# Kernel optimization log

Hardware: AMD Instinct MI355X
Metric: run time of the kernel (lower is better)

The kernel has to match this reference:

```python
import jax, jax.numpy as jnp
import numpy as np
import math

B, S, H, D = 8, 4096, 768, 64  # batch, seq_len, hidden_dim, head_size


def setup_inputs() -> dict:
    key = jax.random.key(0)
    kx, kk, kq, kv, kbk, kbq, kbv = jax.random.split(key, 7)
    s = 1.0 / math.sqrt(H)
    return {
        "x": jax.random.normal(kx, (B, S, H), dtype=jnp.float32),
        "Wk": jax.random.normal(kk, (H, D), dtype=jnp.float32) * s,
        "bk": jax.random.normal(kbk, (D,), dtype=jnp.float32) * s,
        "Wq": jax.random.normal(kq, (H, D), dtype=jnp.float32) * s,
        "bq": jax.random.normal(kbq, (D,), dtype=jnp.float32) * s,
        "Wv": jax.random.normal(kv, (H, D), dtype=jnp.float32) * s,
        "bv": jax.random.normal(kbv, (D,), dtype=jnp.float32) * s,
    }


def reference(x, Wk, bk, Wq, bq, Wv, bv):
    # projections: [B, S, D]
    k = x @ Wk + bk
    q = x @ Wq + bq
    v = x @ Wv + bv
    # full O(S^2) attention scores, as in the original module
    weight = jnp.einsum("bqd,bkd->bqk", q, k)  # [B, S, S]
    causal = jnp.tril(jnp.ones((S, S), dtype=bool))
    # original masks first, then divides by sqrt(head_size); -inf/sqrt = -inf
    weight = jnp.where(causal, weight, -jnp.inf) / math.sqrt(D)
    weight = jax.nn.softmax(weight, axis=-1)
    # dropout p=0.0 (eval-mode reference): identity
    out = jnp.einsum("bqk,bkd->bqd", weight, v)  # [B, S, D]
    return out
```

## Files before the change

### kernel.cpp

```cpp
#include <hip/hip_runtime.h>
#include <hip/hip_bf16.h>
#include <math.h>

#define B_ 8
#define S_ 4096
#define H_ 768
#define D_ 64

typedef __bf16 bf16;
typedef bf16 bf16x8 __attribute__((ext_vector_type(8)));
typedef bf16 bf16x4 __attribute__((ext_vector_type(4)));
typedef float floatx4 __attribute__((ext_vector_type(4)));
typedef short short4v __attribute__((ext_vector_type(4)));

#define S_WAITCNT_VM(N) asm volatile("s_waitcnt vmcnt(" #N ")" ::: "memory")
#define S_BARRIER()     asm volatile("s_barrier" ::: "memory")

__device__ __forceinline__ floatx4 mfma16(bf16x4 a, bf16x4 b, floatx4 c) {
#if __has_builtin(__builtin_amdgcn_mfma_f32_16x16x16_bf16)
    return __builtin_amdgcn_mfma_f32_16x16x16_bf16(a, b, c, 0, 0, 0);
#elif __has_builtin(__builtin_amdgcn_mfma_f32_16x16x16bf16_1k)
    return __builtin_amdgcn_mfma_f32_16x16x16bf16_1k(
        __builtin_bit_cast(short4v, a), __builtin_bit_cast(short4v, b), c, 0, 0, 0);
#else
    asm volatile("v_mfma_f32_16x16x16_bf16 %0, %1, %2, %0"
                 : "+v"(c) : "v"(a), "v"(b));
    return c;
#endif
}

__device__ __forceinline__ int sw_off(int r, int chunk) {
    return r * 128 + ((chunk ^ (r & 7)) << 4);
}
__device__ __forceinline__ int sw_elem(int r, int e) {
    return r * 64 + (((e >> 3) ^ (r & 7)) << 3) + (e & 7);
}

__device__ __forceinline__ void dma16(const void* gsrc, void* ldst) {
    __builtin_amdgcn_global_load_lds(
        (const __attribute__((address_space(1))) unsigned int*)gsrc,
        (__attribute__((address_space(3))) unsigned int*)ldst,
        16, 0, 0);
}

__global__ __launch_bounds__(256) void wtrans_kernel(
    const float* __restrict__ Wq, const float* __restrict__ Wk,
    const float* __restrict__ Wv, bf16* __restrict__ wt)
{
    __shared__ bf16 t_lds[64][72];
    const float* W = (blockIdx.y == 0) ? Wq : (blockIdx.y == 1) ? Wk : Wv;
    bf16* o = wt + ((size_t)blockIdx.y * 12 + blockIdx.x) * 4096;
    const int k0 = blockIdx.x * 64;
    const int tid = threadIdx.x;
    #pragma unroll
    for (int rep = 0; rep < 16; ++rep) {
        int idx = rep * 256 + tid;
        int r = idx >> 6, n = idx & 63;
        t_lds[n][r] = (bf16)W[(size_t)(k0 + r) * D_ + n];
    }
    __syncthreads();
    #pragma unroll
    for (int rep = 0; rep < 16; ++rep) {
        int idx = rep * 256 + tid;
        int n = idx >> 6, kk = idx & 63;
        o[sw_elem(n, kk)] = t_lds[n][kk];
    }
}

__global__ __launch_bounds__(256, 2) void proj_kernel(
    const float* __restrict__ x, const bf16* __restrict__ wt,
    const float* __restrict__ bq, const float* __restrict__ bk,
    const float* __restrict__ bv,
    bf16* __restrict__ qout, bf16* __restrict__ kout, bf16* __restrict__ vtt)
{
    __shared__ bf16  wlds[2][3][4096];
    __shared__ float xlds[2][4096];

    const int tid  = threadIdx.x;
    const int lane = tid & 63;
    const int wave = tid >> 6;
    const int quad = lane >> 4;
    const int c    = lane & 15;
    const int m0   = blockIdx.x * 64;

    auto stageAll = [&](int kt, int buf) {
        #pragma unroll
        for (int w = 0; w < 3; ++w) {
            const bf16* src = wt + (size_t)(w * 12 + kt) * 4096 + wave * 1024 + lane * 8;
            bf16* dst = &wlds[buf][w][wave * 1024 + lane * 8];
            dma16(src, dst);
            dma16(src + 512, dst + 512);
        }
        #pragma unroll
        for (int rep = 0; rep < 4; ++rep) {
            const int ci  = rep * 256 + tid;
            const int row = ci >> 4;
            const int l   = (ci & 15) ^ (row & 15);
            const char* src = (const char*)x
                + ((size_t)(m0 + row) * H_ + kt * 64) * 4 + l * 16;
            dma16(src, (char*)&xlds[buf][0] + ci * 16);
        }
    };

    floatx4 acc[4][3] = {};

    stageAll(0, 0);
    stageAll(1, 1);

    for (int kt = 0; kt < 12; ++kt) {
        if (kt < 11) { S_WAITCNT_VM(10); } else { S_WAITCNT_VM(0); }
        S_BARRIER();
        const int cur = kt & 1;
        #pragma unroll
        for (int s = 0; s < 2; ++s) {
            bf16x8 bfrag[3];
            #pragma unroll
            for (int t = 0; t < 3; ++t) {
                const int g = wave * 3 + t, w = g >> 2, tn = g & 3;
                bfrag[t] = *(const bf16x8*)
                    ((const char*)&wlds[cur][w][0] + sw_off(tn * 16 + c, s * 4 + quad));
            }
            #pragma unroll
            for (int mg = 0; mg < 4; ++mg) {
                const int row = mg * 16 + c;
                const int lc  = s * 8 + quad * 2;
                const char* xb = (const char*)&xlds[cur][0] + row * 256;
                float4 f0 = *(const float4*)(xb + ((lc       ^ (row & 15)) << 4));
                float4 f1 = *(const float4*)(xb + (((lc + 1) ^ (row & 15)) << 4));
                bf16x8 af;
                af[0] = (bf16)f0.x; af[1] = (bf16)f0.y; af[2] = (bf16)f0.z; af[3] = (bf16)f0.w;
                af[4] = (bf16)f1.x; af[5] = (bf16)f1.y; af[6] = (bf16)f1.z; af[7] = (bf16)f1.w;
                #pragma unroll
                for (int t = 0; t < 3; ++t)
                    acc[mg][t] = __builtin_amdgcn_mfma_f32_16x16x32_bf16(
                        af, bfrag[t], acc[mg][t], 0, 0, 0);
            }
        }
        S_BARRIER();
        if (kt < 10) stageAll(kt + 2, cur);
    }

    const int bb = m0 >> 12;
    const int jt = (m0 & 4095) >> 6;
    const size_t tbase = ((size_t)bb * 64 + jt) * 4096;
    #pragma unroll
    for (int t = 0; t < 3; ++t) {
        const int g = wave * 3 + t, w = g >> 2, tn = g & 3;
        const int n = tn * 16 + c;
        const float bias = (w == 0 ? bq : w == 1 ? bk : bv)[n];
        #pragma unroll
        for (int mg = 0; mg < 4; ++mg) {
            const int sl0 = mg * 16 + quad * 4;
            if (w == 0) {
                #pragma unroll
                for (int r = 0; r < 4; ++r)
                    qout[(size_t)(m0 + sl0 + r) * 128 + n] = (bf16)(acc[mg][t][r] + bias);
            } else if (w == 1) {
                #pragma unroll
                for (int r = 0; r < 4; ++r)
                    kout[tbase + sw_elem(sl0 + r, n)] = (bf16)(acc[mg][t][r] + bias);
            } else {
                bf16x4 pk;
                #pragma unroll
                for (int r = 0; r < 4; ++r) pk[r] = (bf16)(acc[mg][t][r] + bias);
                *(bf16x4*)&vtt[tbase + sw_elem(n, sl0)] = pk;
            }
        }
    }
}

__global__ __launch_bounds__(128, 2) void attn_kernel(
    const bf16* __restrict__ q, const bf16* __restrict__ k,
    const bf16* __restrict__ vt, float* __restrict__ out,
    float* __restrict__ opart, float* __restrict__ lpws)
{
    __shared__ bf16 klds[2][4096];
    __shared__ bf16 vlds[2][4096];

    const int tid  = threadIdx.x;
    const int lane = tid & 63;
    const int wave = tid >> 6;
    const int quad = lane >> 4;
    const int c    = lane & 15;
    const int i    = blockIdx.x;
    const int b    = i & 7;

    int qt, j0, jend, half = 0, split = 0;
    if (i < 1024) {
        const int u = i >> 3;
        qt   = 127 - (u >> 1);
        half = u & 1;
        split = 1;
        const int jmax = qt >> 1;
        const int jmid = (jmax + 1) >> 1;
        j0   = half ? jmid : 0;
        jend = half ? jmax : (jmid - 1);
    } else {
        qt   = 63 - ((i - 1024) >> 3);
        j0   = 0;
        jend = qt >> 1;
    }
    const int jmax_diag = qt >> 1;
    const int qrow = qt * 32 + wave * 16;
    const float cl = 0.18033688011112042f;
    const float M2 = 16.0f;

    const bf16* ktile0 = k  + (size_t)b * 64 * 4096;
    const bf16* vtile0 = vt + (size_t)b * 64 * 4096;

    auto stage = [&](const bf16* gsrc, bf16* ldst) {
        const bf16* s = gsrc + wave * 2048 + lane * 8;
        bf16* d = ldst + wave * 2048;
        #pragma unroll
        for (int n = 0; n < 4; ++n) dma16(s + n * 512, d + n * 512);
    };

    bf16x8 qf[2];
    #pragma unroll
    for (int s = 0; s < 2; ++s)
        qf[s] = *(const bf16x8*)
            &q[(size_t)(b * S_ + qrow + c) * 128 + s * 32 + quad * 8];

    floatx4 acc_o[4] = {};
    floatx4 lacc = {0.f, 0.f, 0.f, 0.f};

    stage(ktile0 + (size_t)j0 * 4096, klds[j0 & 1]);
    stage(vtile0 + (size_t)j0 * 4096, vlds[j0 & 1]);
    if (j0 < jend) {
        stage(ktile0 + (size_t)(j0 + 1) * 4096, klds[(j0 + 1) & 1]);
        stage(vtile0 + (size_t)(j0 + 1) * 4096, vlds[(j0 + 1) & 1]);
    }

    #pragma unroll 1
    for (int j = j0; j <= jend; ++j) {
        if (j < jend) { S_WAITCNT_VM(8); } else { S_WAITCNT_VM(0); }
        S_BARRIER();
        const int cur = j & 1;

        floatx4 sa[4] = {};
        #pragma unroll
        for (int s = 0; s < 2; ++s)
            #pragma unroll
            for (int tn = 0; tn < 4; ++tn) {
                bf16x8 kf = *(const bf16x8*)
                    ((const char*)&klds[cur][0] + sw_off(tn * 16 + c, s * 4 + quad));
                sa[tn] = __builtin_amdgcn_mfma_f32_16x16x32_bf16(kf, qf[s], sa[tn], 0, 0, 0);
            }

        bf16x4 vfr[4][4];
        #pragma unroll
        for (int td = 0; td < 4; ++td)
            #pragma unroll
            for (int tn = 0; tn < 4; ++tn)
                vfr[td][tn] = *(const bf16x4*)
                    &vlds[cur][sw_elem(td * 16 + c, tn * 16 + quad * 4)];

        if (j == jmax_diag) {
            #pragma unroll
            for (int tn = 0; tn < 4; ++tn) {
                const int kvb = j * 64 + tn * 16 + quad * 4;
                #pragma unroll
                for (int r = 0; r < 4; ++r)
                    if (kvb + r > qrow + c) sa[tn][r] = -INFINITY;
            }
        }

        #pragma unroll
        for (int tn = 0; tn < 4; ++tn)
            #pragma unroll
            for (int r = 0; r < 4; ++r) {
                float p = __builtin_amdgcn_exp2f(fmaf(sa[tn][r], cl, -M2));
                sa[tn][r] = p;
                lacc[r] += p;
            }

        #pragma unroll
        for (int tn = 0; tn < 4; ++tn) {
            bf16x4 pb;
            #pragma unroll
            for (int r = 0; r < 4; ++r) pb[r] = (bf16)sa[tn][r];
            #pragma unroll
            for (int td = 0; td < 4; ++td)
                acc_o[td] = mfma16(vfr[td][tn], pb, acc_o[td]);
        }

        S_BARRIER();
        if (j + 2 <= jend) {
            stage(ktile0 + (size_t)(j + 2) * 4096, klds[cur]);
            stage(vtile0 + (size_t)(j + 2) * 4096, vlds[cur]);
        }
    }

    float lsum = (lacc[0] + lacc[1]) + (lacc[2] + lacc[3]);
    lsum += __shfl_xor(lsum, 16);
    lsum += __shfl_xor(lsum, 32);

    if (!split) {
        const float rl = 1.0f / lsum;
        #pragma unroll
        for (int td = 0; td < 4; ++td) {
            floatx4 v = acc_o[td] * rl;
            *(float4*)&out[(size_t)(b * S_ + qrow + c) * 64 + td * 16 + quad * 4]
                = *(float4*)&v;
        }
    } else {
        const int tile = qt - 64;
        const int row  = wave * 16 + c;
        float* op = opart + ((((size_t)half * 8 + b) * 64 + tile) * 32) * 64;
        #pragma unroll
        for (int td = 0; td < 4; ++td)
            *(float4*)&op[row * 64 + td * 16 + quad * 4] = *(float4*)&acc_o[td];
        if (quad == 0)
            lpws[(((size_t)half * 8 + b) * 64 + tile) * 32 + row] = lsum;
    }
}

__global__ __launch_bounds__(256) void combine_kernel(
    const float* __restrict__ opart, const float* __restrict__ lpws,
    float* __restrict__ out)
{
    const int b    = blockIdx.x & 7;
    const int tile = blockIdx.x >> 3;
    const int tid  = threadIdx.x;
    const int row  = tid >> 3;
    const int c8   = (tid & 7) * 8;

    const size_t ti = ((size_t)b * 64 + tile) * 32 + row;
    const float rl = 1.0f / (lpws[ti] + lpws[(size_t)8 * 64 * 32 + ti]);

    const size_t oa = (((size_t)b * 64 + tile) * 32 + row) * 64 + c8;
    const size_t ob = (size_t)8 * 64 * 32 * 64 + oa;
    const size_t oo = (size_t)(b * S_ + (64 + tile) * 32 + row) * 64 + c8;
    #pragma unroll
    for (int h = 0; h < 2; ++h) {
        float4 a = *(const float4*)&opart[oa + h * 4];
        float4 bb = *(const float4*)&opart[ob + h * 4];
        float4 o;
        o.x = (a.x + bb.x) * rl; o.y = (a.y + bb.y) * rl;
        o.z = (a.z + bb.z) * rl; o.w = (a.w + bb.w) * rl;
        *(float4*)&out[oo + h * 4] = o;
    }
}

extern "C" void kernel_launch(void* const* d_in, const int* in_sizes, int n_in,
                              void* d_out, int out_size, void* d_ws, size_t ws_size,
                              hipStream_t stream) {
    const float* x  = (const float*)d_in[0];
    const float* Wk = (const float*)d_in[1];
    const float* bk = (const float*)d_in[2];
    const float* Wq = (const float*)d_in[3];
    const float* bq = (const float*)d_in[4];
    const float* Wv = (const float*)d_in[5];
    const float* bv = (const float*)d_in[6];
    float* out = (float*)d_out;

    bf16* q_ws  = (bf16*)d_out;
    bf16* k_ws  = (bf16*)d_ws;
    bf16* vt_ws = k_ws + (size_t)B_ * S_ * D_;
    bf16* wt_ws = vt_ws + (size_t)B_ * S_ * D_;
    float* opart = (float*)(wt_ws + 3 * 12 * 4096);
    float* lpws  = opart + (size_t)2 * 8 * 64 * 32 * 64;

    wtrans_kernel<<<dim3(H_ / 64, 3), 256, 0, stream>>>(Wq, Wk, Wv, wt_ws);
    proj_kernel<<<dim3(B_ * S_ / 64), 256, 0, stream>>>(
        x, wt_ws, bq, bk, bv, q_ws, k_ws, vt_ws);
    attn_kernel<<<dim3(1536), 128, 0, stream>>>(q_ws, k_ws, vt_ws, out, opart, lpws);
    combine_kernel<<<dim3(512), 256, 0, stream>>>(opart, lpws, out);
}
```

Before: 214.5 us.

## Restructure projection kernel: 128-row tiles, x loaded straight to registers, half-K weight staging

The QKV projection kernel now processes 128 rows per block (256 blocks instead of 512), with each wave owning 32 rows and computing all 12 output column tiles for them. x is no longer staged through LDS; each lane loads its fp32 fragments directly from global memory into registers, double-buffered across k-steps. The weights are staged in two large halves (6 k-tiles each) into 144KB of LDS. This is meant to cut LDS traffic and the per-step barriers. In exchange it lowers occupancy to one block per CU, adds a serialized stall while each weight half loads, and raises register pressure.

```diff
diff --git a/kernel.cpp b/kernel.cpp
--- a/kernel.cpp
+++ b/kernel.cpp
@@ -67,104 +67,123 @@
     }
 }
 
-__global__ __launch_bounds__(256, 2) void proj_kernel(
+__global__ __launch_bounds__(256, 1) void proj_kernel(
     const float* __restrict__ x, const bf16* __restrict__ wt,
     const float* __restrict__ bq, const float* __restrict__ bk,
     const float* __restrict__ bv,
     bf16* __restrict__ qout, bf16* __restrict__ kout, bf16* __restrict__ vtt)
 {
-    __shared__ bf16  wlds[2][3][4096];
-    __shared__ float xlds[2][4096];
+    __shared__ bf16 wlds[3][6][4096];
 
     const int tid  = threadIdx.x;
     const int lane = tid & 63;
     const int wave = tid >> 6;
     const int quad = lane >> 4;
     const int c    = lane & 15;
-    const int m0   = blockIdx.x * 64;
-
-    auto stageAll = [&](int kt, int buf) {
-        #pragma unroll
-        for (int w = 0; w < 3; ++w) {
-            const bf16* src = wt + (size_t)(w * 12 + kt) * 4096 + wave * 1024 + lane * 8;
-            bf16* dst = &wlds[buf][w][wave * 1024 + lane * 8];
-            dma16(src, dst);
-            dma16(src + 512, dst + 512);
-        }
-        #pragma unroll
-        for (int rep = 0; rep < 4; ++rep) {
-            const int ci  = rep * 256 + tid;
-            const int row = ci >> 4;
-            const int l   = (ci & 15) ^ (row & 15);
-            const char* src = (const char*)x
-                + ((size_t)(m0 + row) * H_ + kt * 64) * 4 + l * 16;
-            dma16(src, (char*)&xlds[buf][0] + ci * 16);
-        }
+    const int m0   = blockIdx.x * 128;
+
+    auto stageHalf = [&](int h) {
+        #pragma unroll
+        for (int w = 0; w < 3; ++w)
+            #pragma unroll
+            for (int ks = 0; ks < 6; ++ks) {
+                const bf16* src = wt + (size_t)(w * 12 + h * 6 + ks) * 4096 + tid * 8;
+                bf16* dst = &wlds[w][ks][tid * 8];
+                dma16(src, dst);
+                dma16(src + 2048, dst + 2048);
+            }
     };
 
-    floatx4 acc[4][3] = {};
-
-    stageAll(0, 0);
-    stageAll(1, 1);
-
-    for (int kt = 0; kt < 12; ++kt) {
-        if (kt < 11) { S_WAITCNT_VM(10); } else { S_WAITCNT_VM(0); }
-        S_BARRIER();
-        const int cur = kt & 1;
+    floatx4 acc[2][3][4] = {};
+    const float* xr[2];
+    xr[0] = &x[(size_t)(m0 + wave * 32 + c) * H_ + quad * 8];
+    xr[1] = xr[0] + 16 * H_;
+
+    float4 xb[2][2][2][2];
+
+    auto loadx = [&](int kt, int pp) {
+        #pragma unroll
+        for (int rt = 0; rt < 2; ++rt)
+            #pragma unroll
+            for (int s = 0; s < 2; ++s) {
+                const float* p = xr[rt] + kt * 64 + s * 32;
+                xb[pp][rt][s][0] = *(const float4*)p;
+                xb[pp][rt][s][1] = *(const float4*)(p + 4);
+            }
+    };
+
+    auto compute = [&](int kk, int pp) {
         #pragma unroll
         for (int s = 0; s < 2; ++s) {
-            bf16x8 bfrag[3];
-            #pragma unroll
-            for (int t = 0; t < 3; ++t) {
-                const int g = wave * 3 + t, w = g >> 2, tn = g & 3;
-                bfrag[t] = *(const bf16x8*)
-                    ((const char*)&wlds[cur][w][0] + sw_off(tn * 16 + c, s * 4 + quad));
-            }
-            #pragma unroll
-            for (int mg = 0; mg < 4; ++mg) {
-                const int row = mg * 16 + c;
-                const int lc  = s * 8 + quad * 2;
-                const char* xb = (const char*)&xlds[cur][0] + row * 256;
-                float4 f0 = *(const float4*)(xb + ((lc       ^ (row & 15)) << 4));
-                float4 f1 = *(const float4*)(xb + (((lc + 1) ^ (row & 15)) << 4));
+            bf16x8 bfr[3][4];
+            #pragma unroll
+            for (int w = 0; w < 3; ++w)
+                #pragma unroll
+                for (int tn = 0; tn < 4; ++tn)
+                    bfr[w][tn] = *(const bf16x8*)
+                        ((const char*)&wlds[w][kk][0] + sw_off(tn * 16 + c, s * 4 + quad));
+            #pragma unroll
+            for (int rt = 0; rt < 2; ++rt) {
+                float4 f0 = xb[pp][rt][s][0];
+                float4 f1 = xb[pp][rt][s][1];
                 bf16x8 af;
                 af[0] = (bf16)f0.x; af[1] = (bf16)f0.y; af[2] = (bf16)f0.z; af[3] = (bf16)f0.w;
                 af[4] = (bf16)f1.x; af[5] = (bf16)f1.y; af[6] = (bf16)f1.z; af[7] = (bf16)f1.w;
                 #pragma unroll
-                for (int t = 0; t < 3; ++t)
-                    acc[mg][t] = __builtin_amdgcn_mfma_f32_16x16x32_bf16(
-                        af, bfrag[t], acc[mg][t], 0, 0, 0);
-            }
-        }
-        S_BARRIER();
-        if (kt < 10) stageAll(kt + 2, cur);
-    }
-
-    const int bb = m0 >> 12;
-    const int jt = (m0 & 4095) >> 6;
-    const size_t tbase = ((size_t)bb * 64 + jt) * 4096;
-    #pragma unroll
-    for (int t = 0; t < 3; ++t) {
-        const int g = wave * 3 + t, w = g >> 2, tn = g & 3;
-        const int n = tn * 16 + c;
-        const float bias = (w == 0 ? bq : w == 1 ? bk : bv)[n];
-        #pragma unroll
-        for (int mg = 0; mg < 4; ++mg) {
-            const int sl0 = mg * 16 + quad * 4;
-            if (w == 0) {
-                #pragma unroll
-                for (int r = 0; r < 4; ++r)
-                    qout[(size_t)(m0 + sl0 + r) * 128 + n] = (bf16)(acc[mg][t][r] + bias);
-            } else if (w == 1) {
-                #pragma unroll
-                for (int r = 0; r < 4; ++r)
-                    kout[tbase + sw_elem(sl0 + r, n)] = (bf16)(acc[mg][t][r] + bias);
-            } else {
-                bf16x4 pk;
-                #pragma unroll
-                for (int r = 0; r < 4; ++r) pk[r] = (bf16)(acc[mg][t][r] + bias);
-                *(bf16x4*)&vtt[tbase + sw_elem(n, sl0)] = pk;
-            }
+                for (int w = 0; w < 3; ++w)
+                    #pragma unroll
+                    for (int tn = 0; tn < 4; ++tn)
+                        acc[rt][w][tn] = __builtin_amdgcn_mfma_f32_16x16x32_bf16(
+                            af, bfr[w][tn], acc[rt][w][tn], 0, 0, 0);
+            }
+        }
+    };
+
+    stageHalf(0);
+    __syncthreads();
+
+    loadx(0, 0);
+    #pragma unroll
+    for (int kk = 0; kk < 6; ++kk) {
+        if (kk < 5) loadx(kk + 1, (kk + 1) & 1);
+        compute(kk, kk & 1);
+    }
+
+    __syncthreads();
+    stageHalf(1);
+    __syncthreads();
+
+    loadx(6, 0);
+    #pragma unroll
+    for (int kk = 0; kk < 6; ++kk) {
+        if (kk < 5) loadx(7 + kk, (kk + 1) & 1);
+        compute(kk, kk & 1);
+    }
+
+    #pragma unroll
+    for (int rt = 0; rt < 2; ++rt) {
+        const int grow0 = m0 + wave * 32 + rt * 16;
+        const int bb = grow0 >> 12;
+        const int jt = (grow0 & 4095) >> 6;
+        const size_t tbase = ((size_t)bb * 64 + jt) * 4096;
+        const int sl0 = (grow0 & 63) + quad * 4;
+        #pragma unroll
+        for (int tn = 0; tn < 4; ++tn) {
+            const int n = tn * 16 + c;
+            float bqv = bq[n];
+            #pragma unroll
+            for (int r = 0; r < 4; ++r)
+                qout[(size_t)(grow0 + quad * 4 + r) * 128 + n]
+                    = (bf16)(acc[rt][0][tn][r] + bqv);
+            float bkv = bk[n];
+            #pragma unroll
+            for (int r = 0; r < 4; ++r)
+                kout[tbase + sw_elem(sl0 + r, n)] = (bf16)(acc[rt][1][tn][r] + bkv);
+            float bvv = bv[n];
+            bf16x4 pk;
+            #pragma unroll
+            for (int r = 0; r < 4; ++r) pk[r] = (bf16)(acc[rt][2][tn][r] + bvv);
+            *(bf16x4*)&vtt[tbase + sw_elem(n, sl0)] = pk;
         }
     }
 }
@@ -362,7 +381,7 @@
     float* lpws  = opart + (size_t)2 * 8 * 64 * 32 * 64;
 
     wtrans_kernel<<<dim3(H_ / 64, 3), 256, 0, stream>>>(Wq, Wk, Wv, wt_ws);
-    proj_kernel<<<dim3(B_ * S_ / 64), 256, 0, stream>>>(
+    proj_kernel<<<dim3(256), 256, 0, stream>>>(
         x, wt_ws, bq, bk, bv, q_ws, k_ws, vt_ws);
     attn_kernel<<<dim3(1536), 128, 0, stream>>>(q_ws, k_ws, vt_ws, out, opart, lpws);
     combine_kernel<<<dim3(512), 256, 0, stream>>>(opart, lpws, out);
```

Result: slower. 221.7 us (+3.4%).

## Enlarge query tile to 64 rows per block with up to four-way KV split

Applied to the files above, without the earlier changes.

Each wave now handles two 16-row query groups, so every K/V tile loaded into LDS is reused across 64 query rows instead of 32, halving KV traffic per query. Work is split into KV chunks of 16 tiles (up to 4 chunks for long rows), and a reworked combine kernel sums a variable number of partials. This raises register pressure from doubled accumulators, launches fewer blocks (1280), and writes more partial-output data.

```diff
diff --git a/kernel.cpp b/kernel.cpp
--- a/kernel.cpp
+++ b/kernel.cpp
@@ -185,23 +185,16 @@
     const int i    = blockIdx.x;
     const int b    = i & 7;
 
-    int qt, j0, jend, half = 0, split = 0;
-    if (i < 1024) {
-        const int u = i >> 3;
-        qt   = 127 - (u >> 1);
-        half = u & 1;
-        split = 1;
-        const int jmax = qt >> 1;
-        const int jmid = (jmax + 1) >> 1;
-        j0   = half ? jmid : 0;
-        jend = half ? jmax : (jmid - 1);
-    } else {
-        qt   = 63 - ((i - 1024) >> 3);
-        j0   = 0;
-        jend = qt >> 1;
-    }
-    const int jmax_diag = qt >> 1;
-    const int qrow = qt * 32 + wave * 16;
+    const int u = i >> 3;
+    int qt, chunk;
+    if (u < 16)      { qt = u;                 chunk = 0; }
+    else if (u < 48) { qt = 16 + ((u - 16) >> 1); chunk = (u - 16) & 1; }
+    else if (u < 96) { qt = 32 + (u - 48) / 3;    chunk = (u - 48) % 3; }
+    else             { qt = 48 + ((u - 96) >> 2); chunk = (u - 96) & 3; }
+    const int j0    = chunk * 16;
+    const int jend  = min(qt, j0 + 15);
+    const int split = (qt >= 16);
+    const int qrow  = qt * 64 + wave * 32;
     const float cl = 0.18033688011112042f;
     const float M2 = 16.0f;
 
@@ -215,14 +208,16 @@
         for (int n = 0; n < 4; ++n) dma16(s + n * 512, d + n * 512);
     };
 
-    bf16x8 qf[2];
-    #pragma unroll
-    for (int s = 0; s < 2; ++s)
-        qf[s] = *(const bf16x8*)
-            &q[(size_t)(b * S_ + qrow + c) * 128 + s * 32 + quad * 8];
-
-    floatx4 acc_o[4] = {};
-    floatx4 lacc = {0.f, 0.f, 0.f, 0.f};
+    bf16x8 qf[2][2];
+    #pragma unroll
+    for (int mg = 0; mg < 2; ++mg)
+        #pragma unroll
+        for (int s = 0; s < 2; ++s)
+            qf[mg][s] = *(const bf16x8*)
+                &q[(size_t)(b * S_ + qrow + mg * 16 + c) * 128 + s * 32 + quad * 8];
+
+    floatx4 acc_o[2][4] = {};
+    floatx4 lacc[2] = {};
 
     stage(ktile0 + (size_t)j0 * 4096, klds[j0 & 1]);
     stage(vtile0 + (size_t)j0 * 4096, vlds[j0 & 1]);
@@ -237,14 +232,17 @@
         S_BARRIER();
         const int cur = j & 1;
 
-        floatx4 sa[4] = {};
+        floatx4 sa[2][4] = {};
         #pragma unroll
         for (int s = 0; s < 2; ++s)
             #pragma unroll
             for (int tn = 0; tn < 4; ++tn) {
                 bf16x8 kf = *(const bf16x8*)
                     ((const char*)&klds[cur][0] + sw_off(tn * 16 + c, s * 4 + quad));
-                sa[tn] = __builtin_amdgcn_mfma_f32_16x16x32_bf16(kf, qf[s], sa[tn], 0, 0, 0);
+                #pragma unroll
+                for (int mg = 0; mg < 2; ++mg)
+                    sa[mg][tn] = __builtin_amdgcn_mfma_f32_16x16x32_bf16(
+                        kf, qf[mg][s], sa[mg][tn], 0, 0, 0);
             }
 
         bf16x4 vfr[4][4];
@@ -255,34 +253,40 @@
                 vfr[td][tn] = *(const bf16x4*)
                     &vlds[cur][sw_elem(td * 16 + c, tn * 16 + quad * 4)];
 
-        if (j == jmax_diag) {
+        if (j == qt) {
+            #pragma unroll
+            for (int mg = 0; mg < 2; ++mg)
+                #pragma unroll
+                for (int tn = 0; tn < 4; ++tn) {
+                    const int kvb = j * 64 + tn * 16 + quad * 4;
+                    #pragma unroll
+                    for (int r = 0; r < 4; ++r)
+                        if (kvb + r > qrow + mg * 16 + c) sa[mg][tn][r] = -INFINITY;
+                }
+        }
+
+        #pragma unroll
+        for (int mg = 0; mg < 2; ++mg)
+            #pragma unroll
+            for (int tn = 0; tn < 4; ++tn)
+                #pragma unroll
+                for (int r = 0; r < 4; ++r) {
+                    float p = __builtin_amdgcn_exp2f(fmaf(sa[mg][tn][r], cl, -M2));
+                    sa[mg][tn][r] = p;
+                    lacc[mg][r] += p;
+                }
+
+        #pragma unroll
+        for (int mg = 0; mg < 2; ++mg)
             #pragma unroll
             for (int tn = 0; tn < 4; ++tn) {
-                const int kvb = j * 64 + tn * 16 + quad * 4;
-                #pragma unroll
-                for (int r = 0; r < 4; ++r)
-                    if (kvb + r > qrow + c) sa[tn][r] = -INFINITY;
-            }
-        }
-
-        #pragma unroll
-        for (int tn = 0; tn < 4; ++tn)
-            #pragma unroll
-            for (int r = 0; r < 4; ++r) {
-                float p = __builtin_amdgcn_exp2f(fmaf(sa[tn][r], cl, -M2));
-                sa[tn][r] = p;
-                lacc[r] += p;
-            }
-
-        #pragma unroll
-        for (int tn = 0; tn < 4; ++tn) {
-            bf16x4 pb;
-            #pragma unroll
-            for (int r = 0; r < 4; ++r) pb[r] = (bf16)sa[tn][r];
-            #pragma unroll
-            for (int td = 0; td < 4; ++td)
-                acc_o[td] = mfma16(vfr[td][tn], pb, acc_o[td]);
-        }
+                bf16x4 pb;
+                #pragma unroll
+                for (int r = 0; r < 4; ++r) pb[r] = (bf16)sa[mg][tn][r];
+                #pragma unroll
+                for (int td = 0; td < 4; ++td)
+                    acc_o[mg][td] = mfma16(vfr[td][tn], pb, acc_o[mg][td]);
+            }
 
         S_BARRIER();
         if (j + 2 <= jend) {
@@ -291,27 +295,38 @@
         }
     }
 
-    float lsum = (lacc[0] + lacc[1]) + (lacc[2] + lacc[3]);
-    lsum += __shfl_xor(lsum, 16);
-    lsum += __shfl_xor(lsum, 32);
+    float lsum[2];
+    #pragma unroll
+    for (int mg = 0; mg < 2; ++mg) {
+        float l = (lacc[mg][0] + lacc[mg][1]) + (lacc[mg][2] + lacc[mg][3]);
+        l += __shfl_xor(l, 16);
+        l += __shfl_xor(l, 32);
+        lsum[mg] = l;
+    }
 
     if (!split) {
-        const float rl = 1.0f / lsum;
-        #pragma unroll
-        for (int td = 0; td < 4; ++td) {
-            floatx4 v = acc_o[td] * rl;
-            *(float4*)&out[(size_t)(b * S_ + qrow + c) * 64 + td * 16 + quad * 4]
-                = *(float4*)&v;
+        #pragma unroll
+        for (int mg = 0; mg < 2; ++mg) {
+            const float rl = 1.0f / lsum[mg];
+            #pragma unroll
+            for (int td = 0; td < 4; ++td) {
+                floatx4 v = acc_o[mg][td] * rl;
+                *(float4*)&out[(size_t)(b * S_ + qrow + mg * 16 + c) * 64
+                               + td * 16 + quad * 4] = *(float4*)&v;
+            }
         }
     } else {
-        const int tile = qt - 64;
-        const int row  = wave * 16 + c;
-        float* op = opart + ((((size_t)half * 8 + b) * 64 + tile) * 32) * 64;
-        #pragma unroll
-        for (int td = 0; td < 4; ++td)
-            *(float4*)&op[row * 64 + td * 16 + quad * 4] = *(float4*)&acc_o[td];
-        if (quad == 0)
-            lpws[(((size_t)half * 8 + b) * 64 + tile) * 32 + row] = lsum;
+        const size_t pbase = (((size_t)b * 64 + qt) * 4 + chunk) * 4096;
+        #pragma unroll
+        for (int mg = 0; mg < 2; ++mg) {
+            const int row = wave * 32 + mg * 16 + c;
+            #pragma unroll
+            for (int td = 0; td < 4; ++td)
+                *(float4*)&opart[pbase + row * 64 + td * 16 + quad * 4]
+                    = *(float4*)&acc_o[mg][td];
+            if (quad == 0)
+                lpws[(((size_t)b * 64 + qt) * 4 + chunk) * 64 + row] = lsum[mg];
+        }
     }
 }
 
@@ -319,26 +334,30 @@
     const float* __restrict__ opart, const float* __restrict__ lpws,
     float* __restrict__ out)
 {
-    const int b    = blockIdx.x & 7;
-    const int tile = blockIdx.x >> 3;
-    const int tid  = threadIdx.x;
-    const int row  = tid >> 3;
-    const int c8   = (tid & 7) * 8;
-
-    const size_t ti = ((size_t)b * 64 + tile) * 32 + row;
-    const float rl = 1.0f / (lpws[ti] + lpws[(size_t)8 * 64 * 32 + ti]);
-
-    const size_t oa = (((size_t)b * 64 + tile) * 32 + row) * 64 + c8;
-    const size_t ob = (size_t)8 * 64 * 32 * 64 + oa;
-    const size_t oo = (size_t)(b * S_ + (64 + tile) * 32 + row) * 64 + c8;
-    #pragma unroll
-    for (int h = 0; h < 2; ++h) {
-        float4 a = *(const float4*)&opart[oa + h * 4];
-        float4 bb = *(const float4*)&opart[ob + h * 4];
-        float4 o;
-        o.x = (a.x + bb.x) * rl; o.y = (a.y + bb.y) * rl;
-        o.z = (a.z + bb.z) * rl; o.w = (a.w + bb.w) * rl;
-        *(float4*)&out[oo + h * 4] = o;
+    const int bi  = blockIdx.x;
+    const int b   = bi & 7;
+    const int qt  = 16 + (bi >> 3);
+    const int nc  = (qt >> 4) + 1;
+    const int tid = threadIdx.x;
+    const int row = tid >> 2;
+    const int c16 = (tid & 3) * 16;
+
+    const size_t lbase = ((size_t)b * 64 + qt) * 4;
+    float l = 0.f;
+    for (int ch = 0; ch < nc; ++ch) l += lpws[(lbase + ch) * 64 + row];
+    const float rl = 1.0f / l;
+
+    const size_t obase = lbase * 4096 + (size_t)row * 64 + c16;
+    const size_t oo = (size_t)(b * S_ + qt * 64 + row) * 64 + c16;
+    #pragma unroll
+    for (int h = 0; h < 4; ++h) {
+        float4 s = {0.f, 0.f, 0.f, 0.f};
+        for (int ch = 0; ch < nc; ++ch) {
+            float4 a = *(const float4*)&opart[obase + (size_t)ch * 4096 + h * 4];
+            s.x += a.x; s.y += a.y; s.z += a.z; s.w += a.w;
+        }
+        s.x *= rl; s.y *= rl; s.z *= rl; s.w *= rl;
+        *(float4*)&out[oo + h * 4] = s;
     }
 }
 
@@ -359,11 +378,11 @@
     bf16* vt_ws = k_ws + (size_t)B_ * S_ * D_;
     bf16* wt_ws = vt_ws + (size_t)B_ * S_ * D_;
     float* opart = (float*)(wt_ws + 3 * 12 * 4096);
-    float* lpws  = opart + (size_t)2 * 8 * 64 * 32 * 64;
+    float* lpws  = opart + (size_t)8 * 64 * 4 * 4096;
 
     wtrans_kernel<<<dim3(H_ / 64, 3), 256, 0, stream>>>(Wq, Wk, Wv, wt_ws);
     proj_kernel<<<dim3(B_ * S_ / 64), 256, 0, stream>>>(
         x, wt_ws, bq, bk, bv, q_ws, k_ws, vt_ws);
-    attn_kernel<<<dim3(1536), 128, 0, stream>>>(q_ws, k_ws, vt_ws, out, opart, lpws);
-    combine_kernel<<<dim3(512), 256, 0, stream>>>(opart, lpws, out);
-}
+    attn_kernel<<<dim3(1280), 128, 0, stream>>>(q_ws, k_ws, vt_ws, out, opart, lpws);
+    combine_kernel<<<dim3(8 * 48), 256, 0, stream>>>(opart, lpws, out);
+}
```

New measurement: 217.6 us. Within noise of the previous version (+1.5%).

## Preload full x row-tile to LDS as bf16 once in projection kernel

Applied to the files above, without the earlier changes.

The projection kernel now loads the block's whole 64x768 slice of x up front, converts it to bf16 and stores it in a swizzled LDS buffer. This replaces the per-k-step fp32 DMA staging and the repeated float-to-bf16 conversion inside the MFMA loop. Only the weight tiles stay double-buffered through DMA, with the wait counts adjusted to match. LDS use grows to about 120KB, so launch bounds drop to one block per CU. The x load is also no longer overlapped with compute, which adds an exposed latency phase before the main loop.

```diff
diff --git a/kernel.cpp b/kernel.cpp
--- a/kernel.cpp
+++ b/kernel.cpp
@@ -67,14 +67,14 @@
     }
 }
 
-__global__ __launch_bounds__(256, 2) void proj_kernel(
+__global__ __launch_bounds__(256, 1) void proj_kernel(
     const float* __restrict__ x, const bf16* __restrict__ wt,
     const float* __restrict__ bq, const float* __restrict__ bk,
     const float* __restrict__ bv,
     bf16* __restrict__ qout, bf16* __restrict__ kout, bf16* __restrict__ vtt)
 {
-    __shared__ bf16  wlds[2][3][4096];
-    __shared__ float xlds[2][4096];
+    __shared__ bf16 xbf[64 * 768];
+    __shared__ bf16 wlds[2][3][4096];
 
     const int tid  = threadIdx.x;
     const int lane = tid & 63;
@@ -83,7 +83,7 @@
     const int c    = lane & 15;
     const int m0   = blockIdx.x * 64;
 
-    auto stageAll = [&](int kt, int buf) {
+    auto stageW = [&](int kt, int buf) {
         #pragma unroll
         for (int w = 0; w < 3; ++w) {
             const bf16* src = wt + (size_t)(w * 12 + kt) * 4096 + wave * 1024 + lane * 8;
@@ -91,24 +91,30 @@
             dma16(src, dst);
             dma16(src + 512, dst + 512);
         }
-        #pragma unroll
-        for (int rep = 0; rep < 4; ++rep) {
-            const int ci  = rep * 256 + tid;
-            const int row = ci >> 4;
-            const int l   = (ci & 15) ^ (row & 15);
-            const char* src = (const char*)x
-                + ((size_t)(m0 + row) * H_ + kt * 64) * 4 + l * 16;
-            dma16(src, (char*)&xlds[buf][0] + ci * 16);
-        }
     };
 
+    stageW(0, 0);
+    stageW(1, 1);
+
+    #pragma unroll 4
+    for (int rep = 0; rep < 24; ++rep) {
+        const int ci    = rep * 256 + tid;
+        const int row   = ci / 96;
+        const int chunk = ci - row * 96;
+        const float* src = x + ((size_t)(m0 + row) * H_ + chunk * 8);
+        float4 f0 = *(const float4*)src;
+        float4 f1 = *(const float4*)(src + 4);
+        bf16x8 v;
+        v[0] = (bf16)f0.x; v[1] = (bf16)f0.y; v[2] = (bf16)f0.z; v[3] = (bf16)f0.w;
+        v[4] = (bf16)f1.x; v[5] = (bf16)f1.y; v[6] = (bf16)f1.z; v[7] = (bf16)f1.w;
+        *(bf16x8*)&xbf[row * 768 + ((chunk ^ (row & 7)) << 3)] = v;
+    }
+    __syncthreads();
+
     floatx4 acc[4][3] = {};
 
-    stageAll(0, 0);
-    stageAll(1, 1);
-
     for (int kt = 0; kt < 12; ++kt) {
-        if (kt < 11) { S_WAITCNT_VM(10); } else { S_WAITCNT_VM(0); }
+        if (kt >= 2) { if (kt < 11) { S_WAITCNT_VM(6); } else { S_WAITCNT_VM(0); } }
         S_BARRIER();
         const int cur = kt & 1;
         #pragma unroll
@@ -123,13 +129,9 @@
             #pragma unroll
             for (int mg = 0; mg < 4; ++mg) {
                 const int row = mg * 16 + c;
-                const int lc  = s * 8 + quad * 2;
-                const char* xb = (const char*)&xlds[cur][0] + row * 256;
-                float4 f0 = *(const float4*)(xb + ((lc       ^ (row & 15)) << 4));
-                float4 f1 = *(const float4*)(xb + (((lc + 1) ^ (row & 15)) << 4));
-                bf16x8 af;
-                af[0] = (bf16)f0.x; af[1] = (bf16)f0.y; af[2] = (bf16)f0.z; af[3] = (bf16)f0.w;
-                af[4] = (bf16)f1.x; af[5] = (bf16)f1.y; af[6] = (bf16)f1.z; af[7] = (bf16)f1.w;
+                const int chunk = kt * 8 + s * 4 + quad;
+                bf16x8 af = *(const bf16x8*)
+                    &xbf[row * 768 + ((chunk ^ (row & 7)) << 3)];
                 #pragma unroll
                 for (int t = 0; t < 3; ++t)
                     acc[mg][t] = __builtin_amdgcn_mfma_f32_16x16x32_bf16(
@@ -137,7 +139,7 @@
             }
         }
         S_BARRIER();
-        if (kt < 10) stageAll(kt + 2, cur);
+        if (kt < 10) stageW(kt + 2, cur);
     }
 
     const int bb = m0 >> 12;
```

New measurement: 226.9 us. 5.8% more time.
